# Kernel tuning notes

Hardware: AMD Instinct MI355X
Metric: run time of the kernel (lower is better)

The kernel has to match this reference:

```python
import jax, jax.numpy as jnp
import numpy as np

D_MODEL = 1024
N_HEADS = 16
N_KV = N_HEADS // 2
HEAD_DIM = D_MODEL // N_HEADS
HIDDEN = 4 * D_MODEL
B, T = 4, 2048


def setup_inputs() -> dict:
    key = jax.random.key(0)
    ks = jax.random.split(key, 10)
    s = 0.02
    return {
        "x": jax.random.normal(ks[0], (B, T, D_MODEL), dtype=jnp.float32),
        "g1": jnp.ones((D_MODEL,), jnp.float32),
        "g2": jnp.ones((D_MODEL,), jnp.float32),
        "wq": jax.random.normal(ks[1], (D_MODEL, D_MODEL), jnp.float32) * s,
        "wk": jax.random.normal(ks[2], (D_MODEL, N_KV * HEAD_DIM), jnp.float32) * s,
        "wv": jax.random.normal(ks[3], (D_MODEL, N_KV * HEAD_DIM), jnp.float32) * s,
        "wo": jax.random.normal(ks[4], (D_MODEL, D_MODEL), jnp.float32) * s,
        "w1": jax.random.normal(ks[5], (D_MODEL, HIDDEN), jnp.float32) * s,
        "w2": jax.random.normal(ks[6], (D_MODEL, HIDDEN), jnp.float32) * s,
        "w3": jax.random.normal(ks[7], (HIDDEN, D_MODEL), jnp.float32) * s,
    }


def _rmsnorm(x, g, eps=1e-6):
    return x * jax.lax.rsqrt(jnp.mean(x * x, axis=-1, keepdims=True) + eps) * g


def _rope(q, k):
    # q: [B,H,T,d], k: [B,Hkv,T,d]; half-split rotary as in the torch RoPE
    d = q.shape[-1]
    t = jnp.arange(q.shape[2], dtype=jnp.float32)
    inv_freq = 1.0 / (10000.0 ** (jnp.arange(0, d, 2, dtype=jnp.float32) / d))
    freqs = t[:, None] * inv_freq[None, :]            # [T, d/2]
    cos = jnp.cos(freqs)[None, None, :, :]
    sin = jnp.sin(freqs)[None, None, :, :]

    def rot(x):
        x1, x2 = jnp.split(x, 2, axis=-1)
        return jnp.concatenate([x1 * cos - x2 * sin, x2 * cos + x1 * sin], axis=-1)

    return rot(q), rot(k)


def reference(x, g1, g2, wq, wk, wv, wo, w1, w2, w3):
    Bb, Tt, C = x.shape
    h = _rmsnorm(x, g1)
    q = (h @ wq).reshape(Bb, Tt, N_HEADS, HEAD_DIM).transpose(0, 2, 1, 3)
    k = (h @ wk).reshape(Bb, Tt, N_KV, HEAD_DIM).transpose(0, 2, 1, 3)
    v = (h @ wv).reshape(Bb, Tt, N_KV, HEAD_DIM).transpose(0, 2, 1, 3)
    q, k = _rope(q, k)
    rep = N_HEADS // N_KV
    k = jnp.repeat(k, rep, axis=1)
    v = jnp.repeat(v, rep, axis=1)
    att = jnp.einsum("bhtd,bhsd->bhts", q, k) / np.sqrt(HEAD_DIM)
    causal = jnp.tril(jnp.ones((Tt, Tt), dtype=bool))
    att = jnp.where(causal[None, None], att, -jnp.inf)
    att = jax.nn.softmax(att, axis=-1)
    out = jnp.einsum("bhts,bhsd->bhtd", att, v)
    out = out.transpose(0, 2, 1, 3).reshape(Bb, Tt, C) @ wo
    x = x + out
    h2 = _rmsnorm(x, g2)
    ffn = (jax.nn.silu(h2 @ w1) * (h2 @ w2)) @ w3
    return x + ffn
```

## Files before the change

kernel.cpp:

```cpp
#include <hip/hip_runtime.h>
#include <cstdint>

typedef __attribute__((ext_vector_type(8))) short bfrag;
typedef __attribute__((ext_vector_type(4))) float f4;

typedef __attribute__((address_space(1))) const void* gas_t;
typedef __attribute__((address_space(3))) void* las_t;

__device__ __forceinline__ void gload16(const void* g, void* l) {
  __builtin_amdgcn_global_load_lds((gas_t)g, (las_t)l, 16, 0, 0);
}

__device__ __forceinline__ unsigned short f2bf(float f) {
  union { float f; unsigned u; } v; v.f = f;
  unsigned r = v.u + 0x7fffu + ((v.u >> 16) & 1u);
  return (unsigned short)(r >> 16);
}
__device__ __forceinline__ float bf2f(unsigned short b) {
  union { unsigned u; float f; } v; v.u = ((unsigned)b) << 16;
  return v.f;
}
__device__ __forceinline__ unsigned cvt_pk_bf16(float lo, float hi) {
  unsigned r;
  asm("v_cvt_pk_bf16_f32 %0, %1, %2" : "=v"(r) : "v"(lo), "v"(hi));
  return r;
}

__device__ __forceinline__ void xcd_swz(int& bx, int& by) {
  int gx = gridDim.x;
  int lid = blockIdx.y * gx + blockIdx.x;
  int nwg = gx * gridDim.y;
  int swz = (lid & 7) * (nwg >> 3) + (lid >> 3);
  bx = swz % gx;
  by = swz / gx;
}

__global__ __launch_bounds__(256) void tconv_k(const float* __restrict__ in,
                                               unsigned short* __restrict__ out,
                                               int R, int C) {
  __shared__ unsigned short t[32][33];
  const int c0 = blockIdx.x * 32, r0 = blockIdx.y * 32;
  const int tid = threadIdx.x;
#pragma unroll
  for (int p = 0; p < 4; p++) {
    int flat = p * 256 + tid;
    int r = flat >> 5, c = flat & 31;
    t[r][c] = f2bf(in[(size_t)(r0 + r) * C + c0 + c]);
  }
  __syncthreads();
#pragma unroll
  for (int p = 0; p < 4; p++) {
    int flat = p * 256 + tid;
    int cc = flat >> 5, rr = flat & 31;
    out[(size_t)(c0 + cc) * R + r0 + rr] = t[rr][cc];
  }
}

__global__ __launch_bounds__(256) void rmsnorm_k(const float* __restrict__ x,
                                                 const float* __restrict__ g,
                                                 unsigned short* __restrict__ out) {
  const int row = blockIdx.x, tid = threadIdx.x;
  const float4 v = ((const float4*)(x + (size_t)row * 1024))[tid];
  float ss = v.x * v.x + v.y * v.y + v.z * v.z + v.w * v.w;
#pragma unroll
  for (int off = 1; off < 64; off <<= 1) ss += __shfl_xor(ss, off);
  __shared__ float red[4];
  if ((tid & 63) == 0) red[tid >> 6] = ss;
  __syncthreads();
  float tot = red[0] + red[1] + red[2] + red[3];
  float sc = rsqrtf(tot * (1.0f / 1024.0f) + 1e-6f);
  const float4 gv = ((const float4*)g)[tid];
  ushort4 o;
  o.x = f2bf(v.x * sc * gv.x);
  o.y = f2bf(v.y * sc * gv.y);
  o.z = f2bf(v.z * sc * gv.z);
  o.w = f2bf(v.w * sc * gv.w);
  ((ushort4*)out)[(size_t)row * 256 + tid] = o;
}

template <int MODE>
__global__ __launch_bounds__(256) void gemm_k(const unsigned short* __restrict__ A,
                                              const unsigned short* __restrict__ Bt,
                                              int M, int N, int K,
                                              void* __restrict__ Cout,
                                              const float* __restrict__ resid) {
  __shared__ unsigned short As[128 * 32];
  __shared__ unsigned short Bs[128 * 32];
  const int tid = threadIdx.x;
  const int wid = tid >> 6, lane = tid & 63;
  const int l15 = lane & 15, l4 = lane >> 4;
  int bx, by;
  xcd_swz(bx, by);
  const int brow = bx * 128, bcol = by * 128;
  const int wr = (wid >> 1) * 64, wc = (wid & 1) * 64;
  const int x15 = l15 & 3;
  f4 acc[4][4];
#pragma unroll
  for (int m = 0; m < 4; m++)
#pragma unroll
    for (int n = 0; n < 4; n++) acc[m][n] = (f4){0.f, 0.f, 0.f, 0.f};

  for (int k0 = 0; k0 < K; k0 += 32) {
#pragma unroll
    for (int c = 0; c < 2; c++) {
      int slot = c * 256 + tid;
      int r = slot >> 2, cp = slot & 3;
      int sc = (cp ^ (r & 3)) * 8;
      gload16(A + (size_t)(brow + r) * K + k0 + sc, &As[slot * 8]);
      gload16(Bt + (size_t)(bcol + r) * K + k0 + sc, &Bs[slot * 8]);
    }
    __syncthreads();
    bfrag a[4], b[4];
#pragma unroll
    for (int m = 0; m < 4; m++)
      a[m] = *(const bfrag*)&As[(wr + m * 16 + l15) * 32 + (l4 ^ x15) * 8];
#pragma unroll
    for (int n = 0; n < 4; n++)
      b[n] = *(const bfrag*)&Bs[(wc + n * 16 + l15) * 32 + (l4 ^ x15) * 8];
#pragma unroll
    for (int m = 0; m < 4; m++)
#pragma unroll
      for (int n = 0; n < 4; n++)
        acc[m][n] = __builtin_amdgcn_mfma_f32_16x16x32_bf16(a[m], b[n], acc[m][n], 0, 0, 0);
    __syncthreads();
  }
#pragma unroll
  for (int m = 0; m < 4; m++)
#pragma unroll
    for (int n = 0; n < 4; n++)
#pragma unroll
      for (int j = 0; j < 4; j++) {
        int r = brow + wr + m * 16 + l4 * 4 + j;
        int col = bcol + wc + n * 16 + l15;
        if (MODE == 0) {
          ((unsigned short*)Cout)[(size_t)r * N + col] = f2bf(acc[m][n][j]);
        } else {
          ((float*)Cout)[(size_t)r * N + col] = acc[m][n][j] + resid[(size_t)r * N + col];
        }
      }
}

__global__ __launch_bounds__(256, 2) void ffn1_k(const unsigned short* __restrict__ A,
                                                 const unsigned short* __restrict__ B1t,
                                                 const unsigned short* __restrict__ B2t,
                                                 unsigned short* __restrict__ G,
                                                 int M, int N, int K) {
  __shared__ unsigned short As[128 * 32];
  __shared__ unsigned short B1s[64 * 32];
  __shared__ unsigned short B2s[64 * 32];
  const int tid = threadIdx.x;
  const int wid = tid >> 6, lane = tid & 63;
  const int l15 = lane & 15, l4 = lane >> 4;
  int bx, by;
  xcd_swz(bx, by);
  const int brow = bx * 128, bcol = by * 64;
  const int wr = (wid >> 1) * 64, wc = (wid & 1) * 32;
  const int x15 = l15 & 3;
  f4 acc1[4][2], acc2[4][2];
#pragma unroll
  for (int m = 0; m < 4; m++)
#pragma unroll
    for (int n = 0; n < 2; n++) {
      acc1[m][n] = (f4){0.f, 0.f, 0.f, 0.f};
      acc2[m][n] = (f4){0.f, 0.f, 0.f, 0.f};
    }

  for (int k0 = 0; k0 < K; k0 += 32) {
#pragma unroll
    for (int p = 0; p < 2; p++) {
      int slot = p * 256 + tid;
      int r = slot >> 2, cp = slot & 3;
      int sc = (cp ^ (r & 3)) * 8;
      gload16(A + (size_t)(brow + r) * K + k0 + sc, &As[slot * 8]);
    }
    {
      int r = tid >> 2, cp = tid & 3;
      int sc = (cp ^ (r & 3)) * 8;
      gload16(B1t + (size_t)(bcol + r) * K + k0 + sc, &B1s[tid * 8]);
      gload16(B2t + (size_t)(bcol + r) * K + k0 + sc, &B2s[tid * 8]);
    }
    __syncthreads();
    bfrag a[4], b1[2], b2[2];
#pragma unroll
    for (int m = 0; m < 4; m++)
      a[m] = *(const bfrag*)&As[(wr + m * 16 + l15) * 32 + (l4 ^ x15) * 8];
#pragma unroll
    for (int n = 0; n < 2; n++) {
      b1[n] = *(const bfrag*)&B1s[(wc + n * 16 + l15) * 32 + (l4 ^ x15) * 8];
      b2[n] = *(const bfrag*)&B2s[(wc + n * 16 + l15) * 32 + (l4 ^ x15) * 8];
    }
#pragma unroll
    for (int m = 0; m < 4; m++)
#pragma unroll
      for (int n = 0; n < 2; n++) {
        acc1[m][n] = __builtin_amdgcn_mfma_f32_16x16x32_bf16(a[m], b1[n], acc1[m][n], 0, 0, 0);
        acc2[m][n] = __builtin_amdgcn_mfma_f32_16x16x32_bf16(a[m], b2[n], acc2[m][n], 0, 0, 0);
      }
    __syncthreads();
  }
#pragma unroll
  for (int m = 0; m < 4; m++)
#pragma unroll
    for (int n = 0; n < 2; n++)
#pragma unroll
      for (int j = 0; j < 4; j++) {
        int r = brow + wr + m * 16 + l4 * 4 + j;
        int col = bcol + wc + n * 16 + l15;
        float v1 = acc1[m][n][j], v2 = acc2[m][n][j];
        float sg = v1 / (1.0f + expf(-v1));
        G[(size_t)r * N + col] = f2bf(sg * v2);
      }
}

__global__ __launch_bounds__(256) void rope_k(unsigned short* __restrict__ qkv) {
  int idx = blockIdx.x * 256 + threadIdx.x;
  int i = idx & 31;
  int rest = idx >> 5;
  int head = rest % 24;
  int row = rest / 24;
  int t = row & 2047;
  int col = (head < 16) ? (head * 64 + i) : (1024 + (head - 16) * 64 + i);
  size_t base = (size_t)row * 2048 + col;
  float ang = (float)t * exp2f(-(float)i * (13.287712379549449f / 32.0f));
  float s, c;
  sincosf(ang, &s, &c);
  float a = bf2f(qkv[base]), b = bf2f(qkv[base + 32]);
  qkv[base] = f2bf(a * c - b * s);
  qkv[base + 32] = f2bf(b * c + a * s);
}

__global__ __launch_bounds__(256) void vtrans_k(const unsigned short* __restrict__ qkv,
                                                unsigned short* __restrict__ vt) {
  __shared__ unsigned short t[64][65];
  const int t0 = blockIdx.x * 64;
  const int bkh = blockIdx.y;
  const int b = bkh >> 3, kh = bkh & 7;
  const int tid = threadIdx.x;
#pragma unroll
  for (int p = 0; p < 16; p++) {
    int flat = p * 256 + tid;
    int tl = flat >> 6, dl = flat & 63;
    t[tl][dl] = qkv[(size_t)(b * 2048 + t0 + tl) * 2048 + 1536 + kh * 64 + dl];
  }
  __syncthreads();
#pragma unroll
  for (int p = 0; p < 16; p++) {
    int flat = p * 256 + tid;
    int dl = flat >> 6, tl = flat & 63;
    vt[((size_t)(b * 8 + kh) * 64 + dl) * 2048 + t0 + tl] = t[tl][dl];
  }
}

__global__ __launch_bounds__(256) void attn_k(const unsigned short* __restrict__ qkv,
                                              const unsigned short* __restrict__ vt,
                                              unsigned short* __restrict__ out) {
  const int blk = blockIdx.x;
  const int bkh = blk & 31;
  const int tile = 63 - (blk >> 5);
  const int b = bkh >> 3, kh = bkh & 7;
  const int tid = threadIdx.x;
  const int w = tid >> 6, lane = tid & 63, l15 = lane & 15, l4 = lane >> 4;
  const int h = kh * 2 + (w >> 1);
  const int t0w = tile * 32 + (w & 1) * 16;
  const int thi = tile * 32 + 31;

  __shared__ unsigned short KT[2][4096];
  __shared__ unsigned short VT[2][4096];
  __shared__ unsigned short P[4][16 * 72];
  unsigned short* Pw = &P[w][0];

  const unsigned short* qbase = qkv + (size_t)(b * 2048 + t0w + l15) * 2048 + h * 64;
  bfrag q0 = *(const bfrag*)(qbase + l4 * 8);
  bfrag q1 = *(const bfrag*)(qbase + 32 + l4 * 8);

  float mrun = -1e30f, lsum = 0.f;
  f4 o[4];
#pragma unroll
  for (int d = 0; d < 4; d++) o[d] = (f4){0.f, 0.f, 0.f, 0.f};

  const unsigned short* vbase = vt + (size_t)(b * 8 + kh) * 64 * 2048;
  const float sc2 = 0.125f * 1.4426950408889634f;

  auto STAGE = [&](int buf, int s0) {
#pragma unroll
    for (int p = 0; p < 2; ++p) {
      int c = p * 256 + w * 64 + lane;
      int r = c >> 3, sl = (c & 7) ^ (r & 7);
      gload16(qkv + (size_t)(b * 2048 + s0 + r) * 2048 + 1024 + kh * 64 + sl * 8,
              &KT[buf][(p * 256 + w * 64) * 8]);
      gload16(vbase + (size_t)r * 2048 + s0 + sl * 8,
              &VT[buf][(p * 256 + w * 64) * 8]);
    }
  };

  STAGE(0, 0);
  int cur = 0;
  for (int s0 = 0; s0 <= thi; s0 += 64) {
    if (s0 + 64 <= thi) {
      STAGE(cur ^ 1, s0 + 64);
      asm volatile("s_waitcnt vmcnt(4)" ::: "memory");
    } else {
      asm volatile("s_waitcnt vmcnt(0)" ::: "memory");
    }
    __builtin_amdgcn_s_barrier();

    f4 sa[4];
#pragma unroll
    for (int sub = 0; sub < 4; ++sub) {
      int rb = sub * 16 + l15;
      int x = rb & 7;
      bfrag k0 = *(const bfrag*)&KT[cur][(rb * 8 + (l4 ^ x)) * 8];
      bfrag k1 = *(const bfrag*)&KT[cur][(rb * 8 + ((l4 + 4) ^ x)) * 8];
      f4 z = (f4){0.f, 0.f, 0.f, 0.f};
      z = __builtin_amdgcn_mfma_f32_16x16x32_bf16(k0, q0, z, 0, 0, 0);
      z = __builtin_amdgcn_mfma_f32_16x16x32_bf16(k1, q1, z, 0, 0, 0);
      sa[sub] = z;
    }
    const int t = t0w + l15;
    float pv[4][4];
    float mloc = -1e30f;
#pragma unroll
    for (int sub = 0; sub < 4; ++sub)
#pragma unroll
      for (int j = 0; j < 4; ++j) {
        int s = s0 + sub * 16 + l4 * 4 + j;
        float v = sa[sub][j] * sc2;
        if (s > t) v = -1e30f;
        pv[sub][j] = v;
        mloc = fmaxf(mloc, v);
      }
    mloc = fmaxf(mloc, __shfl_xor(mloc, 16));
    mloc = fmaxf(mloc, __shfl_xor(mloc, 32));
    float mnew = fmaxf(mrun, mloc);
    float al = __builtin_amdgcn_exp2f(mrun - mnew);
    mrun = mnew;
    float rs = 0.f;
#pragma unroll
    for (int sub = 0; sub < 4; ++sub)
#pragma unroll
      for (int j = 0; j < 4; ++j) {
        float e = __builtin_amdgcn_exp2f(pv[sub][j] - mnew);
        pv[sub][j] = e;
        rs += e;
      }
    rs += __shfl_xor(rs, 16);
    rs += __shfl_xor(rs, 32);
    lsum = lsum * al + rs;
#pragma unroll
    for (int d = 0; d < 4; d++)
#pragma unroll
      for (int j = 0; j < 4; j++) o[d][j] *= al;

#pragma unroll
    for (int sub = 0; sub < 4; ++sub) {
      uint2 u;
      u.x = cvt_pk_bf16(pv[sub][0], pv[sub][1]);
      u.y = cvt_pk_bf16(pv[sub][2], pv[sub][3]);
      *(uint2*)&Pw[l15 * 72 + sub * 16 + l4 * 4] = u;
    }
#pragma unroll
    for (int sh = 0; sh < 2; ++sh) {
      bfrag pf = *(const bfrag*)&Pw[l15 * 72 + sh * 32 + l4 * 8];
#pragma unroll
      for (int dblk = 0; dblk < 4; ++dblk) {
        int d = dblk * 16 + l15;
        bfrag vf = *(const bfrag*)&VT[cur][(d * 8 + ((sh * 4 + l4) ^ (d & 7))) * 8];
        o[dblk] = __builtin_amdgcn_mfma_f32_16x16x32_bf16(vf, pf, o[dblk], 0, 0, 0);
      }
    }
    asm volatile("s_waitcnt lgkmcnt(0)" ::: "memory");
    __builtin_amdgcn_s_barrier();
    cur ^= 1;
  }
  float inv = 1.0f / lsum;
#pragma unroll
  for (int d = 0; d < 4; d++) {
    ushort4 st;
    st.x = f2bf(o[d][0] * inv);
    st.y = f2bf(o[d][1] * inv);
    st.z = f2bf(o[d][2] * inv);
    st.w = f2bf(o[d][3] * inv);
    *(ushort4*)&out[(size_t)(b * 2048 + t0w + l15) * 1024 + h * 64 + d * 16 + l4 * 4] = st;
  }
}

extern "C" void kernel_launch(void* const* d_in, const int* in_sizes, int n_in,
                              void* d_out, int out_size, void* d_ws, size_t ws_size,
                              hipStream_t stream) {
  const float* x = (const float*)d_in[0];
  const float* g1 = (const float*)d_in[1];
  const float* g2 = (const float*)d_in[2];
  const float* wq = (const float*)d_in[3];
  const float* wk = (const float*)d_in[4];
  const float* wv = (const float*)d_in[5];
  const float* wo = (const float*)d_in[6];
  const float* w1 = (const float*)d_in[7];
  const float* w2 = (const float*)d_in[8];
  const float* w3 = (const float*)d_in[9];

  const size_t MB = 1024 * 1024;
  uint8_t* ws = (uint8_t*)d_ws;
  unsigned short* wqkv_t = (unsigned short*)(ws);
  unsigned short* wo_t = (unsigned short*)(ws + 4 * MB);
  unsigned short* w1_t = (unsigned short*)(ws + 6 * MB);
  unsigned short* w2_t = (unsigned short*)(ws + 14 * MB);
  unsigned short* w3_t = (unsigned short*)(ws + 22 * MB);
  unsigned short* hbuf = (unsigned short*)(ws + 30 * MB);
  unsigned short* qkv = (unsigned short*)(ws + 46 * MB);
  unsigned short* vt = (unsigned short*)(ws + 78 * MB);
  unsigned short* attn_o = (unsigned short*)(ws + 86 * MB);
  unsigned short* gbuf = (unsigned short*)(ws + 46 * MB);
  float* x1 = (float*)(ws + 110 * MB);

  tconv_k<<<dim3(32, 32), 256, 0, stream>>>(wq, wqkv_t, 1024, 1024);
  tconv_k<<<dim3(16, 32), 256, 0, stream>>>(wk, wqkv_t + (size_t)1024 * 1024, 1024, 512);
  tconv_k<<<dim3(16, 32), 256, 0, stream>>>(wv, wqkv_t + (size_t)1536 * 1024, 1024, 512);
  tconv_k<<<dim3(32, 32), 256, 0, stream>>>(wo, wo_t, 1024, 1024);
  tconv_k<<<dim3(128, 32), 256, 0, stream>>>(w1, w1_t, 1024, 4096);
  tconv_k<<<dim3(128, 32), 256, 0, stream>>>(w2, w2_t, 1024, 4096);
  tconv_k<<<dim3(32, 128), 256, 0, stream>>>(w3, w3_t, 4096, 1024);

  rmsnorm_k<<<8192, 256, 0, stream>>>(x, g1, hbuf);
  gemm_k<0><<<dim3(64, 16), 256, 0, stream>>>(hbuf, wqkv_t, 8192, 2048, 1024, qkv, nullptr);
  rope_k<<<24576, 256, 0, stream>>>(qkv);
  vtrans_k<<<dim3(32, 32), 256, 0, stream>>>(qkv, vt);
  attn_k<<<2048, 256, 0, stream>>>(qkv, vt, attn_o);
  gemm_k<1><<<dim3(64, 8), 256, 0, stream>>>(attn_o, wo_t, 8192, 1024, 1024, x1, x);
  rmsnorm_k<<<8192, 256, 0, stream>>>(x1, g2, hbuf);
  ffn1_k<<<dim3(64, 64), 256, 0, stream>>>(hbuf, w1_t, w2_t, gbuf, 8192, 4096, 1024);
  gemm_k<1><<<dim3(64, 8), 256, 0, stream>>>(gbuf, w3_t, 8192, 1024, 4096, (float*)d_out, x1);
}
```

Measured before the change: 648.5 us.

## Split ffn1 gate/up GEMMs across warp groups with 128x128 tiles

The fused SwiGLU GEMM now runs 512-thread blocks over a 128x128 output tile. Half the waves compute the w1 product and half the w2 product, each holding 4x4 accumulators, so every A tile is reused across twice as many columns. The w2 results are passed through LDS as bf16 so the w1 waves can apply SiLU and the multiply. This halves the grid and the A reloads, at the cost of an extra LDS exchange, a bf16 rounding of the up projection, and higher per-block resource use.

```diff
diff --git a/kernel.cpp b/kernel.cpp
--- a/kernel.cpp
+++ b/kernel.cpp
@@ -140,76 +140,80 @@
       }
 }
 
-__global__ __launch_bounds__(256, 2) void ffn1_k(const unsigned short* __restrict__ A,
-                                                 const unsigned short* __restrict__ B1t,
-                                                 const unsigned short* __restrict__ B2t,
-                                                 unsigned short* __restrict__ G,
-                                                 int M, int N, int K) {
-  __shared__ unsigned short As[128 * 32];
-  __shared__ unsigned short B1s[64 * 32];
-  __shared__ unsigned short B2s[64 * 32];
+__global__ __launch_bounds__(512) void ffn1_k(const unsigned short* __restrict__ A,
+                                              const unsigned short* __restrict__ B1t,
+                                              const unsigned short* __restrict__ B2t,
+                                              unsigned short* __restrict__ G,
+                                              int M, int N, int K) {
+  __shared__ unsigned short LB[16640];
+  unsigned short* As = LB;
+  unsigned short* B1s = LB + 4096;
+  unsigned short* B2s = LB + 8192;
   const int tid = threadIdx.x;
-  const int wid = tid >> 6, lane = tid & 63;
+  const int w = tid >> 6, lane = tid & 63;
   const int l15 = lane & 15, l4 = lane >> 4;
   int bx, by;
   xcd_swz(bx, by);
-  const int brow = bx * 128, bcol = by * 64;
-  const int wr = (wid >> 1) * 64, wc = (wid & 1) * 32;
+  const int brow = bx * 128, bcol = by * 128;
+  const int wq = w & 3;
+  const int wr = (wq >> 1) * 64, wc = (wq & 1) * 64;
   const int x15 = l15 & 3;
-  f4 acc1[4][2], acc2[4][2];
+  f4 acc[4][4];
 #pragma unroll
   for (int m = 0; m < 4; m++)
 #pragma unroll
-    for (int n = 0; n < 2; n++) {
-      acc1[m][n] = (f4){0.f, 0.f, 0.f, 0.f};
-      acc2[m][n] = (f4){0.f, 0.f, 0.f, 0.f};
-    }
+    for (int n = 0; n < 4; n++) acc[m][n] = (f4){0.f, 0.f, 0.f, 0.f};
 
   for (int k0 = 0; k0 < K; k0 += 32) {
-#pragma unroll
-    for (int p = 0; p < 2; p++) {
-      int slot = p * 256 + tid;
-      int r = slot >> 2, cp = slot & 3;
-      int sc = (cp ^ (r & 3)) * 8;
-      gload16(A + (size_t)(brow + r) * K + k0 + sc, &As[slot * 8]);
-    }
     {
       int r = tid >> 2, cp = tid & 3;
       int sc = (cp ^ (r & 3)) * 8;
+      gload16(A + (size_t)(brow + r) * K + k0 + sc, &As[tid * 8]);
       gload16(B1t + (size_t)(bcol + r) * K + k0 + sc, &B1s[tid * 8]);
       gload16(B2t + (size_t)(bcol + r) * K + k0 + sc, &B2s[tid * 8]);
     }
     __syncthreads();
-    bfrag a[4], b1[2], b2[2];
+    const unsigned short* Bs = (w < 4) ? B1s : B2s;
+    bfrag a[4], b[4];
 #pragma unroll
     for (int m = 0; m < 4; m++)
       a[m] = *(const bfrag*)&As[(wr + m * 16 + l15) * 32 + (l4 ^ x15) * 8];
 #pragma unroll
-    for (int n = 0; n < 2; n++) {
-      b1[n] = *(const bfrag*)&B1s[(wc + n * 16 + l15) * 32 + (l4 ^ x15) * 8];
-      b2[n] = *(const bfrag*)&B2s[(wc + n * 16 + l15) * 32 + (l4 ^ x15) * 8];
-    }
-#pragma unroll
-    for (int m = 0; m < 4; m++)
-#pragma unroll
-      for (int n = 0; n < 2; n++) {
-        acc1[m][n] = __builtin_amdgcn_mfma_f32_16x16x32_bf16(a[m], b1[n], acc1[m][n], 0, 0, 0);
-        acc2[m][n] = __builtin_amdgcn_mfma_f32_16x16x32_bf16(a[m], b2[n], acc2[m][n], 0, 0, 0);
-      }
+    for (int n = 0; n < 4; n++)
+      b[n] = *(const bfrag*)&Bs[(wc + n * 16 + l15) * 32 + (l4 ^ x15) * 8];
+#pragma unroll
+    for (int m = 0; m < 4; m++)
+#pragma unroll
+      for (int n = 0; n < 4; n++)
+        acc[m][n] = __builtin_amdgcn_mfma_f32_16x16x32_bf16(a[m], b[n], acc[m][n], 0, 0, 0);
     __syncthreads();
   }
-#pragma unroll
-  for (int m = 0; m < 4; m++)
-#pragma unroll
-    for (int n = 0; n < 2; n++)
-#pragma unroll
-      for (int j = 0; j < 4; j++) {
-        int r = brow + wr + m * 16 + l4 * 4 + j;
-        int col = bcol + wc + n * 16 + l15;
-        float v1 = acc1[m][n][j], v2 = acc2[m][n][j];
-        float sg = v1 / (1.0f + expf(-v1));
-        G[(size_t)r * N + col] = f2bf(sg * v2);
-      }
+
+  if (w >= 4) {
+#pragma unroll
+    for (int m = 0; m < 4; m++)
+#pragma unroll
+      for (int n = 0; n < 4; n++)
+#pragma unroll
+        for (int j = 0; j < 4; j++)
+          LB[(wr + m * 16 + l4 * 4 + j) * 130 + wc + n * 16 + l15] = f2bf(acc[m][n][j]);
+  }
+  __syncthreads();
+  if (w < 4) {
+#pragma unroll
+    for (int m = 0; m < 4; m++)
+#pragma unroll
+      for (int n = 0; n < 4; n++)
+#pragma unroll
+        for (int j = 0; j < 4; j++) {
+          int rr = wr + m * 16 + l4 * 4 + j;
+          int cc = wc + n * 16 + l15;
+          float v1 = acc[m][n][j];
+          float v2 = bf2f(LB[rr * 130 + cc]);
+          float sg = v1 / (1.0f + expf(-v1));
+          G[(size_t)(brow + rr) * N + bcol + cc] = f2bf(sg * v2);
+        }
+  }
 }
 
 __global__ __launch_bounds__(256) void rope_k(unsigned short* __restrict__ qkv) {
@@ -427,6 +431,6 @@
   attn_k<<<2048, 256, 0, stream>>>(qkv, vt, attn_o);
   gemm_k<1><<<dim3(64, 8), 256, 0, stream>>>(attn_o, wo_t, 8192, 1024, 1024, x1, x);
   rmsnorm_k<<<8192, 256, 0, stream>>>(x1, g2, hbuf);
-  ffn1_k<<<dim3(64, 64), 256, 0, stream>>>(hbuf, w1_t, w2_t, gbuf, 8192, 4096, 1024);
+  ffn1_k<<<dim3(64, 32), 512, 0, stream>>>(hbuf, w1_t, w2_t, gbuf, 8192, 4096, 1024);
   gemm_k<1><<<dim3(64, 8), 256, 0, stream>>>(gbuf, w3_t, 8192, 1024, 4096, (float*)d_out, x1);
 }
```

New measurement: 628.7 us. 1.03x faster.
